# Optimization experiments

Measured on AMD Instinct MI355X. Metric: run time of the kernel, lower is better.

The kernel has to match this reference:

```python
import jax, jax.numpy as jnp
import numpy as np

B, S, D = 2, 1024, 1024      # batch, seq_len, d_model
E, K, FF = 8, 2, 2048        # num_experts, top_k, dim_feedforward


def setup_inputs() -> dict:
    key = jax.random.key(0)
    k1, k2, k3, k4 = jax.random.split(key, 4)
    x = jax.random.normal(k1, (B, S, D), dtype=jnp.float32)
    router_w = jax.random.normal(k2, (E, D), dtype=jnp.float32) * 0.02   # nn.Linear(d_model, num_experts).weight
    w1 = jax.random.normal(k3, (E, FF, D), dtype=jnp.float32) * 0.02     # per-expert nn.Linear(d, ff).weight
    w2 = jax.random.normal(k4, (E, D, FF), dtype=jnp.float32) * 0.02     # per-expert nn.Linear(ff, d).weight
    return {"x": x, "router_w": router_w, "w1": w1, "w2": w2}


def reference(x, router_w, w1, w2):
    # Router: logits -> softmax -> top-k -> renormalize
    logits = jnp.einsum('bsd,ed->bse', x, router_w)
    router_probs = jax.nn.softmax(logits, axis=-1)                       # [B,S,E]
    topk_weights, topk_indices = jax.lax.top_k(router_probs, K)          # [B,S,K]
    topk_weights = topk_weights / topk_weights.sum(axis=-1, keepdims=True)
    # Combine weight per (token, expert): sum of top-k weights routed to that expert
    combine = (jax.nn.one_hot(topk_indices, E, dtype=x.dtype) * topk_weights[..., None]).sum(axis=-2)  # [B,S,E]
    # Experts: SwiGLU-less SiLU MLP per expert, applied densely then masked by combine weights.
    h = jax.nn.silu(jnp.einsum('bsd,efd->bsef', x, w1))                  # [B,S,E,FF]
    y = jnp.einsum('bsef,edf->bsed', h, w2)                              # [B,S,E,D]
    output = jnp.einsum('bsed,bse->bsd', y, combine)                     # [B,S,D]
    return output, router_probs, topk_indices, topk_weights
```

## Files before the change

kernel.cpp:

```cpp
#include <hip/hip_runtime.h>
#include <hip/hip_bf16.h>

#define TOKENS 2048
#define DMODEL 1024
#define NEXP 8
#define TOPK 2
#define FFDIM 2048
#define MAXSLOTS 5120
#define MTILES (MAXSLOTS / 128)

typedef __bf16 bf16_t;
typedef __bf16 bf16x8 __attribute__((ext_vector_type(8)));
typedef __bf16 bf16x4 __attribute__((ext_vector_type(4)));
typedef float f32x4 __attribute__((ext_vector_type(4)));

#define OUT_PROBS (TOKENS * DMODEL)
#define OUT_IDX (OUT_PROBS + TOKENS * NEXP)
#define OUT_W (OUT_IDX + TOKENS * TOPK)

#define WS_TOKE 0
#define WS_TOKW 16384
#define WS_OFFS 32768
#define WS_ROWTOK 33024
#define WS_SLOTOF 53504
#define WS_XB 131072
#define WS_H 4325376
#define WS_Y 25296896
#define WS_WB 35782656

__device__ __forceinline__ void async16(const bf16_t* g, bf16_t* l) {
    __builtin_amdgcn_global_load_lds(
        (const __attribute__((address_space(1))) unsigned int*)g,
        (__attribute__((address_space(3))) unsigned int*)l, 16, 0, 0);
}

__global__ __launch_bounds__(256) void k_cast(const float* __restrict__ src,
                                              bf16_t* __restrict__ dst) {
    const size_t i = ((size_t)blockIdx.x * 256 + threadIdx.x) * 8;
    float4 a = *(const float4*)&src[i];
    float4 b = *(const float4*)&src[i + 4];
    bf16x8 v;
    v[0] = (bf16_t)a.x; v[1] = (bf16_t)a.y; v[2] = (bf16_t)a.z; v[3] = (bf16_t)a.w;
    v[4] = (bf16_t)b.x; v[5] = (bf16_t)b.y; v[6] = (bf16_t)b.z; v[7] = (bf16_t)b.w;
    *(bf16x8*)&dst[i] = v;
}

__global__ __launch_bounds__(256) void k_router(
        const float* __restrict__ x, const float* __restrict__ rw,
        float* __restrict__ out, int* __restrict__ tok_e, float* __restrict__ tok_w,
        bf16_t* __restrict__ xb) {
    __shared__ float s_rw[NEXP * DMODEL];
    const float4* rw4 = (const float4*)rw;
    float4* s4 = (float4*)s_rw;
#pragma unroll
    for (int i = 0; i < (NEXP * DMODEL / 4) / 256; ++i)
        s4[i * 256 + threadIdx.x] = rw4[i * 256 + threadIdx.x];
    __syncthreads();

    const int wave = threadIdx.x >> 6;
    const int lane = threadIdx.x & 63;
    const int t = blockIdx.x * 4 + wave;

    float acc[NEXP];
#pragma unroll
    for (int e = 0; e < NEXP; ++e) acc[e] = 0.f;
    const float4* xr = (const float4*)(x + (size_t)t * DMODEL);
#pragma unroll
    for (int j = 0; j < DMODEL / 256; ++j) {
        float4 xv = xr[j * 64 + lane];
        bf16x4 xc;
        xc[0] = (bf16_t)xv.x; xc[1] = (bf16_t)xv.y; xc[2] = (bf16_t)xv.z; xc[3] = (bf16_t)xv.w;
        *(bf16x4*)&xb[(size_t)t * DMODEL + (j * 64 + lane) * 4] = xc;
#pragma unroll
        for (int e = 0; e < NEXP; ++e) {
            const float4 rv = *(const float4*)&s_rw[e * DMODEL + (j * 64 + lane) * 4];
            acc[e] += xv.x * rv.x + xv.y * rv.y + xv.z * rv.z + xv.w * rv.w;
        }
    }
#pragma unroll
    for (int off = 32; off > 0; off >>= 1) {
#pragma unroll
        for (int e = 0; e < NEXP; ++e) acc[e] += __shfl_xor(acc[e], off);
    }

    if (lane == 0) {
        float m = acc[0];
#pragma unroll
        for (int e = 1; e < NEXP; ++e) m = fmaxf(m, acc[e]);
        float p[NEXP];
        float sum = 0.f;
#pragma unroll
        for (int e = 0; e < NEXP; ++e) { p[e] = expf(acc[e] - m); sum += p[e]; }
#pragma unroll
        for (int e = 0; e < NEXP; ++e) p[e] = p[e] / sum;
        int i0 = 0;
#pragma unroll
        for (int e = 1; e < NEXP; ++e) if (p[e] > p[i0]) i0 = e;
        int i1 = (i0 == 0) ? 1 : 0;
#pragma unroll
        for (int e = 0; e < NEXP; ++e) if (e != i0 && p[e] > p[i1]) i1 = e;
        float w0 = p[i0], w1 = p[i1];
        float s2 = w0 + w1;
        float w0n = w0 / s2, w1n = w1 / s2;
#pragma unroll
        for (int e = 0; e < NEXP; ++e) out[OUT_PROBS + (size_t)t * NEXP + e] = p[e];
        out[OUT_IDX + (size_t)t * TOPK + 0] = (float)i0;
        out[OUT_IDX + (size_t)t * TOPK + 1] = (float)i1;
        out[OUT_W + (size_t)t * TOPK + 0] = w0n;
        out[OUT_W + (size_t)t * TOPK + 1] = w1n;
        tok_e[t * 2 + 0] = i0;
        tok_e[t * 2 + 1] = i1;
        tok_w[t * 2 + 0] = w0n;
        tok_w[t * 2 + 1] = w1n;
    }
}

__global__ void k_finalize(const int* __restrict__ tok_e,
                           int* __restrict__ offs, int* __restrict__ row_tok,
                           int* __restrict__ slot_of) {
    __shared__ int cnt[NEXP];
    __shared__ int fill[NEXP];
    __shared__ int soff[NEXP + 1];
    const int tid = threadIdx.x;
    if (tid < NEXP) { cnt[tid] = 0; fill[tid] = 0; }
    __syncthreads();
    for (int i = tid; i < TOKENS * 2; i += 256) atomicAdd(&cnt[tok_e[i]], 1);
    __syncthreads();
    if (tid == 0) {
        int o = 0;
        for (int e = 0; e < NEXP; ++e) {
            soff[e] = o;
            o += (cnt[e] + 127) & ~127;
        }
        soff[NEXP] = o;
    }
    __syncthreads();
    if (tid <= NEXP) offs[tid] = soff[tid];
    for (int i = tid; i < MAXSLOTS; i += 256) row_tok[i] = -1;
    __syncthreads();
    for (int i = tid; i < TOKENS * 2; i += 256) {
        int e = tok_e[i];
        int pos = atomicAdd(&fill[e], 1);
        int slot = soff[e] + pos;
        row_tok[slot] = i >> 1;
        slot_of[i] = slot;
    }
}

__global__ __launch_bounds__(256, 2) void k_gemm1(
        const bf16_t* __restrict__ xb, const bf16_t* __restrict__ w1b,
        const int* __restrict__ offs, const int* __restrict__ row_tok,
        bf16_t* __restrict__ H) {
    const int m0 = blockIdx.y * 128;
    if (m0 >= offs[NEXP]) return;
    int e = 0;
    while (m0 >= offs[e + 1]) ++e;
    const int n0 = blockIdx.x * 128;

    __shared__ __align__(16) bf16_t As[2][128 * 64];
    __shared__ __align__(16) bf16_t Bs[2][128 * 64];

    const int tid = threadIdx.x;
    const int wid = tid >> 6, lane = tid & 63;
    const int wr = wid >> 1, wc = wid & 1;
    const int lr = lane & 15, ls = lane >> 4;

    const int rq = tid >> 3;
    const int jx = (tid & 7) ^ (rq & 7);
    const bf16_t* asrc[4];
    const bf16_t* bsrc[4];
#pragma unroll
    for (int q = 0; q < 4; ++q) {
        const int r = q * 32 + rq;
        int tok = row_tok[m0 + r];
        if (tok < 0) tok = 0;
        asrc[q] = xb + (size_t)tok * DMODEL + jx * 8;
        bsrc[q] = w1b + ((size_t)e * FFDIM + n0 + r) * DMODEL + jx * 8;
    }

    f32x4 acc[4][4];
#pragma unroll
    for (int mi = 0; mi < 4; ++mi)
#pragma unroll
        for (int ni = 0; ni < 4; ++ni) acc[mi][ni] = (f32x4){0.f, 0.f, 0.f, 0.f};

    const int NK = DMODEL / 64;

#define STAGE1(b, kt)                                      \
    {                                                      \
        bf16_t* Ad = &As[b][wid * 512];                    \
        bf16_t* Bd = &Bs[b][wid * 512];                    \
        _Pragma("unroll") for (int q = 0; q < 4; ++q) {    \
            async16(asrc[q] + (kt) * 64, Ad + q * 2048);   \
            async16(bsrc[q] + (kt) * 64, Bd + q * 2048);   \
        }                                                  \
    }

    int buf = 0;
    STAGE1(0, 0);
    __syncthreads();
    for (int kt = 0; kt < NK; ++kt) {
        if (kt + 1 < NK) STAGE1(buf ^ 1, kt + 1);
#pragma unroll
        for (int kk = 0; kk < 2; ++kk) {
            const int sA = ((kk << 2) + ls) ^ (lr & 7);
            bf16x8 af[4], bv[4];
#pragma unroll
            for (int mi = 0; mi < 4; ++mi)
                af[mi] = *(const bf16x8*)&As[buf][(wr * 64 + mi * 16 + lr) * 64 + sA * 8];
#pragma unroll
            for (int ni = 0; ni < 4; ++ni)
                bv[ni] = *(const bf16x8*)&Bs[buf][(wc * 64 + ni * 16 + lr) * 64 + sA * 8];
#pragma unroll
            for (int mi = 0; mi < 4; ++mi)
#pragma unroll
                for (int ni = 0; ni < 4; ++ni)
                    acc[mi][ni] = __builtin_amdgcn_mfma_f32_16x16x32_bf16(af[mi], bv[ni], acc[mi][ni], 0, 0, 0);
        }
        __syncthreads();
        buf ^= 1;
    }
#undef STAGE1

#pragma unroll
    for (int mi = 0; mi < 4; ++mi) {
        const int rowL = m0 + wr * 64 + mi * 16 + ls * 4;
#pragma unroll
        for (int ni = 0; ni < 4; ++ni) {
            const int colL = n0 + wc * 64 + ni * 16 + lr;
#pragma unroll
            for (int v = 0; v < 4; ++v) {
                float val = acc[mi][ni][v];
                H[(size_t)(rowL + v) * FFDIM + colL] = (bf16_t)(val / (1.f + expf(-val)));
            }
        }
    }
}

__global__ __launch_bounds__(256, 3) void k_gemm2(
        const bf16_t* __restrict__ H, const bf16_t* __restrict__ w2b,
        const int* __restrict__ offs, bf16_t* __restrict__ Y) {
    const int m0 = blockIdx.y * 128;
    if (m0 >= offs[NEXP]) return;
    int e = 0;
    while (m0 >= offs[e + 1]) ++e;
    const int n0 = blockIdx.x * 64;

    __shared__ __align__(16) bf16_t As[2][128 * 64];
    __shared__ __align__(16) bf16_t Bs[2][64 * 64];

    const int tid = threadIdx.x;
    const int wid = tid >> 6, lane = tid & 63;
    const int wr = wid >> 1, wc = wid & 1;
    const int lr = lane & 15, ls = lane >> 4;

    const int rq = tid >> 3;
    const int jx = (tid & 7) ^ (rq & 7);
    const bf16_t* asrc[4];
    const bf16_t* bsrc[2];
#pragma unroll
    for (int q = 0; q < 4; ++q)
        asrc[q] = H + (size_t)(m0 + q * 32 + rq) * FFDIM + jx * 8;
#pragma unroll
    for (int q = 0; q < 2; ++q)
        bsrc[q] = w2b + ((size_t)e * DMODEL + n0 + q * 32 + rq) * FFDIM + jx * 8;

    f32x4 acc[4][2];
#pragma unroll
    for (int mi = 0; mi < 4; ++mi)
#pragma unroll
        for (int ni = 0; ni < 2; ++ni) acc[mi][ni] = (f32x4){0.f, 0.f, 0.f, 0.f};

    const int NK = FFDIM / 64;

#define STAGE2(b, kt)                                      \
    {                                                      \
        bf16_t* Ad = &As[b][wid * 512];                    \
        bf16_t* Bd = &Bs[b][wid * 512];                    \
        _Pragma("unroll") for (int q = 0; q < 4; ++q)      \
            async16(asrc[q] + (kt) * 64, Ad + q * 2048);   \
        _Pragma("unroll") for (int q = 0; q < 2; ++q)      \
            async16(bsrc[q] + (kt) * 64, Bd + q * 2048);   \
    }

    int buf = 0;
    STAGE2(0, 0);
    __syncthreads();
    for (int kt = 0; kt < NK; ++kt) {
        if (kt + 1 < NK) STAGE2(buf ^ 1, kt + 1);
#pragma unroll
        for (int kk = 0; kk < 2; ++kk) {
            const int sA = ((kk << 2) + ls) ^ (lr & 7);
            bf16x8 af[4], bv[2];
#pragma unroll
            for (int mi = 0; mi < 4; ++mi)
                af[mi] = *(const bf16x8*)&As[buf][(wr * 64 + mi * 16 + lr) * 64 + sA * 8];
#pragma unroll
            for (int ni = 0; ni < 2; ++ni)
                bv[ni] = *(const bf16x8*)&Bs[buf][(wc * 32 + ni * 16 + lr) * 64 + sA * 8];
#pragma unroll
            for (int mi = 0; mi < 4; ++mi)
#pragma unroll
                for (int ni = 0; ni < 2; ++ni)
                    acc[mi][ni] = __builtin_amdgcn_mfma_f32_16x16x32_bf16(af[mi], bv[ni], acc[mi][ni], 0, 0, 0);
        }
        __syncthreads();
        buf ^= 1;
    }
#undef STAGE2

#pragma unroll
    for (int mi = 0; mi < 4; ++mi) {
        const int rowL = m0 + wr * 64 + mi * 16 + ls * 4;
#pragma unroll
        for (int ni = 0; ni < 2; ++ni) {
            const int colL = n0 + wc * 32 + ni * 16 + lr;
#pragma unroll
            for (int v = 0; v < 4; ++v)
                Y[(size_t)(rowL + v) * DMODEL + colL] = (bf16_t)acc[mi][ni][v];
        }
    }
}

__global__ __launch_bounds__(256) void k_combine(
        const bf16_t* __restrict__ Y, const int* __restrict__ slot_of,
        const float* __restrict__ tok_w, float* __restrict__ out) {
    const int t = blockIdx.x;
    const int c = threadIdx.x * 4;
    const int s0 = slot_of[t * 2 + 0], s1 = slot_of[t * 2 + 1];
    const float w0 = tok_w[t * 2 + 0], w1 = tok_w[t * 2 + 1];
    bf16x4 y0 = *(const bf16x4*)&Y[(size_t)s0 * DMODEL + c];
    bf16x4 y1 = *(const bf16x4*)&Y[(size_t)s1 * DMODEL + c];
    float4 o;
    o.x = w0 * (float)y0[0] + w1 * (float)y1[0];
    o.y = w0 * (float)y0[1] + w1 * (float)y1[1];
    o.z = w0 * (float)y0[2] + w1 * (float)y1[2];
    o.w = w0 * (float)y0[3] + w1 * (float)y1[3];
    *(float4*)&out[(size_t)t * DMODEL + c] = o;
}

extern "C" void kernel_launch(void* const* d_in, const int* in_sizes, int n_in,
                              void* d_out, int out_size, void* d_ws, size_t ws_size,
                              hipStream_t stream) {
    const float* x = (const float*)d_in[0];
    const float* rw = (const float*)d_in[1];
    const float* w1 = (const float*)d_in[2];
    const float* w2 = (const float*)d_in[3];
    float* out = (float*)d_out;
    char* ws = (char*)d_ws;

    int* tok_e = (int*)(ws + WS_TOKE);
    float* tok_w = (float*)(ws + WS_TOKW);
    int* offs = (int*)(ws + WS_OFFS);
    int* row_tok = (int*)(ws + WS_ROWTOK);
    int* slot_of = (int*)(ws + WS_SLOTOF);
    bf16_t* xb = (bf16_t*)(ws + WS_XB);
    bf16_t* H = (bf16_t*)(ws + WS_H);
    bf16_t* Yb = (bf16_t*)(ws + WS_Y);
    bf16_t* wb = (bf16_t*)(ws + WS_WB);

    const int WCAST_BLOCKS = (NEXP * FFDIM * DMODEL) / (8 * 256);

    k_router<<<TOKENS / 4, 256, 0, stream>>>(x, rw, out, tok_e, tok_w, xb);
    k_finalize<<<1, 256, 0, stream>>>(tok_e, offs, row_tok, slot_of);
    k_cast<<<WCAST_BLOCKS, 256, 0, stream>>>(w1, wb);
    k_gemm1<<<dim3(FFDIM / 128, MTILES), 256, 0, stream>>>(xb, wb, offs, row_tok, H);
    k_cast<<<WCAST_BLOCKS, 256, 0, stream>>>(w2, wb);
    k_gemm2<<<dim3(DMODEL / 64, MTILES), 256, 0, stream>>>(H, wb, offs, Yb);
    k_combine<<<TOKENS, 256, 0, stream>>>(Yb, slot_of, tok_w, out);
}
```

Measured before the change: 254.9 us.

## Fuse fp32-to-bf16 weight conversion into expert GEMM B-tile loads

Removes the separate weight cast kernels and instead has both expert GEMMs load fp32 weight tiles into registers, convert to bf16, and write them swizzled into shared memory. This avoids writing and re-reading a full bf16 copy of each weight tensor. In exchange, each M-tile re-reads fp32 weights (twice the bytes of bf16). The B path also becomes synchronous register staging with a full vmcnt wait, which adds register pressure and weakens the async pipelining.

```diff
diff --git a/kernel.cpp b/kernel.cpp
--- a/kernel.cpp
+++ b/kernel.cpp
@@ -26,7 +26,6 @@
 #define WS_XB 131072
 #define WS_H 4325376
 #define WS_Y 25296896
-#define WS_WB 35782656
 
 __device__ __forceinline__ void async16(const bf16_t* g, bf16_t* l) {
     __builtin_amdgcn_global_load_lds(
@@ -34,15 +33,11 @@
         (__attribute__((address_space(3))) unsigned int*)l, 16, 0, 0);
 }
 
-__global__ __launch_bounds__(256) void k_cast(const float* __restrict__ src,
-                                              bf16_t* __restrict__ dst) {
-    const size_t i = ((size_t)blockIdx.x * 256 + threadIdx.x) * 8;
-    float4 a = *(const float4*)&src[i];
-    float4 b = *(const float4*)&src[i + 4];
+__device__ __forceinline__ bf16x8 cvt8(float4 a, float4 b) {
     bf16x8 v;
     v[0] = (bf16_t)a.x; v[1] = (bf16_t)a.y; v[2] = (bf16_t)a.z; v[3] = (bf16_t)a.w;
     v[4] = (bf16_t)b.x; v[5] = (bf16_t)b.y; v[6] = (bf16_t)b.z; v[7] = (bf16_t)b.w;
-    *(bf16x8*)&dst[i] = v;
+    return v;
 }
 
 __global__ __launch_bounds__(256) void k_router(
@@ -148,7 +143,7 @@
 }
 
 __global__ __launch_bounds__(256, 2) void k_gemm1(
-        const bf16_t* __restrict__ xb, const bf16_t* __restrict__ w1b,
+        const bf16_t* __restrict__ xb, const float* __restrict__ w1,
         const int* __restrict__ offs, const int* __restrict__ row_tok,
         bf16_t* __restrict__ H) {
     const int m0 = blockIdx.y * 128;
@@ -168,15 +163,14 @@
     const int rq = tid >> 3;
     const int jx = (tid & 7) ^ (rq & 7);
     const bf16_t* asrc[4];
-    const bf16_t* bsrc[4];
 #pragma unroll
     for (int q = 0; q < 4; ++q) {
-        const int r = q * 32 + rq;
-        int tok = row_tok[m0 + r];
+        int tok = row_tok[m0 + q * 32 + rq];
         if (tok < 0) tok = 0;
         asrc[q] = xb + (size_t)tok * DMODEL + jx * 8;
-        bsrc[q] = w1b + ((size_t)e * FFDIM + n0 + r) * DMODEL + jx * 8;
-    }
+    }
+    const int rowB = tid >> 1, hB = tid & 1;
+    const float* brow = w1 + ((size_t)e * FFDIM + n0 + rowB) * DMODEL + hB * 32;
 
     f32x4 acc[4][4];
 #pragma unroll
@@ -185,22 +179,31 @@
         for (int ni = 0; ni < 4; ++ni) acc[mi][ni] = (f32x4){0.f, 0.f, 0.f, 0.f};
 
     const int NK = DMODEL / 64;
-
-#define STAGE1(b, kt)                                      \
-    {                                                      \
-        bf16_t* Ad = &As[b][wid * 512];                    \
-        bf16_t* Bd = &Bs[b][wid * 512];                    \
-        _Pragma("unroll") for (int q = 0; q < 4; ++q) {    \
-            async16(asrc[q] + (kt) * 64, Ad + q * 2048);   \
-            async16(bsrc[q] + (kt) * 64, Bd + q * 2048);   \
-        }                                                  \
-    }
+    float4 bb[8];
+
+#define G1_AISSUE(b, kt)                                                     \
+    _Pragma("unroll") for (int q = 0; q < 4; ++q)                            \
+        async16(asrc[q] + (kt) * 64, &As[b][wid * 512] + q * 2048);
+#define G1_BLOAD(kt)                                                         \
+    _Pragma("unroll") for (int i = 0; i < 8; ++i)                            \
+        bb[i] = *(const float4*)(brow + (kt) * 64 + i * 4);
+#define G1_BWRITE(b)                                                         \
+    _Pragma("unroll") for (int s = 0; s < 4; ++s)                            \
+        *(bf16x8*)&Bs[b][rowB * 64 + (((hB << 2) + s) ^ (rowB & 7)) * 8] =   \
+            cvt8(bb[2 * s], bb[2 * s + 1]);
+
+    G1_BLOAD(0);
+    G1_AISSUE(0, 0);
+    asm volatile("s_waitcnt vmcnt(0)" ::: "memory");
+    G1_BWRITE(0);
+    __syncthreads();
 
     int buf = 0;
-    STAGE1(0, 0);
-    __syncthreads();
     for (int kt = 0; kt < NK; ++kt) {
-        if (kt + 1 < NK) STAGE1(buf ^ 1, kt + 1);
+        if (kt + 1 < NK) {
+            G1_BLOAD(kt + 1);
+            G1_AISSUE(buf ^ 1, kt + 1);
+        }
 #pragma unroll
         for (int kk = 0; kk < 2; ++kk) {
             const int sA = ((kk << 2) + ls) ^ (lr & 7);
@@ -217,10 +220,16 @@
                 for (int ni = 0; ni < 4; ++ni)
                     acc[mi][ni] = __builtin_amdgcn_mfma_f32_16x16x32_bf16(af[mi], bv[ni], acc[mi][ni], 0, 0, 0);
         }
+        if (kt + 1 < NK) {
+            asm volatile("s_waitcnt vmcnt(0)" ::: "memory");
+            G1_BWRITE(buf ^ 1);
+        }
         __syncthreads();
         buf ^= 1;
     }
-#undef STAGE1
+#undef G1_AISSUE
+#undef G1_BLOAD
+#undef G1_BWRITE
 
 #pragma unroll
     for (int mi = 0; mi < 4; ++mi) {
@@ -238,7 +247,7 @@
 }
 
 __global__ __launch_bounds__(256, 3) void k_gemm2(
-        const bf16_t* __restrict__ H, const bf16_t* __restrict__ w2b,
+        const bf16_t* __restrict__ H, const float* __restrict__ w2,
         const int* __restrict__ offs, bf16_t* __restrict__ Y) {
     const int m0 = blockIdx.y * 128;
     if (m0 >= offs[NEXP]) return;
@@ -257,13 +266,11 @@
     const int rq = tid >> 3;
     const int jx = (tid & 7) ^ (rq & 7);
     const bf16_t* asrc[4];
-    const bf16_t* bsrc[2];
 #pragma unroll
     for (int q = 0; q < 4; ++q)
         asrc[q] = H + (size_t)(m0 + q * 32 + rq) * FFDIM + jx * 8;
-#pragma unroll
-    for (int q = 0; q < 2; ++q)
-        bsrc[q] = w2b + ((size_t)e * DMODEL + n0 + q * 32 + rq) * FFDIM + jx * 8;
+    const int rowB = tid >> 2, qB = tid & 3;
+    const float* brow = w2 + ((size_t)e * DMODEL + n0 + rowB) * FFDIM + qB * 16;
 
     f32x4 acc[4][2];
 #pragma unroll
@@ -272,22 +279,31 @@
         for (int ni = 0; ni < 2; ++ni) acc[mi][ni] = (f32x4){0.f, 0.f, 0.f, 0.f};
 
     const int NK = FFDIM / 64;
-
-#define STAGE2(b, kt)                                      \
-    {                                                      \
-        bf16_t* Ad = &As[b][wid * 512];                    \
-        bf16_t* Bd = &Bs[b][wid * 512];                    \
-        _Pragma("unroll") for (int q = 0; q < 4; ++q)      \
-            async16(asrc[q] + (kt) * 64, Ad + q * 2048);   \
-        _Pragma("unroll") for (int q = 0; q < 2; ++q)      \
-            async16(bsrc[q] + (kt) * 64, Bd + q * 2048);   \
-    }
+    float4 cb[4];
+
+#define G2_AISSUE(b, kt)                                                     \
+    _Pragma("unroll") for (int q = 0; q < 4; ++q)                            \
+        async16(asrc[q] + (kt) * 64, &As[b][wid * 512] + q * 2048);
+#define G2_BLOAD(kt)                                                         \
+    _Pragma("unroll") for (int i = 0; i < 4; ++i)                            \
+        cb[i] = *(const float4*)(brow + (kt) * 64 + i * 4);
+#define G2_BWRITE(b)                                                         \
+    _Pragma("unroll") for (int s = 0; s < 2; ++s)                            \
+        *(bf16x8*)&Bs[b][rowB * 64 + (((qB << 1) + s) ^ (rowB & 7)) * 8] =   \
+            cvt8(cb[2 * s], cb[2 * s + 1]);
+
+    G2_BLOAD(0);
+    G2_AISSUE(0, 0);
+    asm volatile("s_waitcnt vmcnt(0)" ::: "memory");
+    G2_BWRITE(0);
+    __syncthreads();
 
     int buf = 0;
-    STAGE2(0, 0);
-    __syncthreads();
     for (int kt = 0; kt < NK; ++kt) {
-        if (kt + 1 < NK) STAGE2(buf ^ 1, kt + 1);
+        if (kt + 1 < NK) {
+            G2_BLOAD(kt + 1);
+            G2_AISSUE(buf ^ 1, kt + 1);
+        }
 #pragma unroll
         for (int kk = 0; kk < 2; ++kk) {
             const int sA = ((kk << 2) + ls) ^ (lr & 7);
@@ -304,10 +320,16 @@
                 for (int ni = 0; ni < 2; ++ni)
                     acc[mi][ni] = __builtin_amdgcn_mfma_f32_16x16x32_bf16(af[mi], bv[ni], acc[mi][ni], 0, 0, 0);
         }
+        if (kt + 1 < NK) {
+            asm volatile("s_waitcnt vmcnt(0)" ::: "memory");
+            G2_BWRITE(buf ^ 1);
+        }
         __syncthreads();
         buf ^= 1;
     }
-#undef STAGE2
+#undef G2_AISSUE
+#undef G2_BLOAD
+#undef G2_BWRITE
 
 #pragma unroll
     for (int mi = 0; mi < 4; ++mi) {
@@ -357,15 +379,10 @@
     bf16_t* xb = (bf16_t*)(ws + WS_XB);
     bf16_t* H = (bf16_t*)(ws + WS_H);
     bf16_t* Yb = (bf16_t*)(ws + WS_Y);
-    bf16_t* wb = (bf16_t*)(ws + WS_WB);
-
-    const int WCAST_BLOCKS = (NEXP * FFDIM * DMODEL) / (8 * 256);
 
     k_router<<<TOKENS / 4, 256, 0, stream>>>(x, rw, out, tok_e, tok_w, xb);
     k_finalize<<<1, 256, 0, stream>>>(tok_e, offs, row_tok, slot_of);
-    k_cast<<<WCAST_BLOCKS, 256, 0, stream>>>(w1, wb);
-    k_gemm1<<<dim3(FFDIM / 128, MTILES), 256, 0, stream>>>(xb, wb, offs, row_tok, H);
-    k_cast<<<WCAST_BLOCKS, 256, 0, stream>>>(w2, wb);
-    k_gemm2<<<dim3(DMODEL / 64, MTILES), 256, 0, stream>>>(H, wb, offs, Yb);
+    k_gemm1<<<dim3(FFDIM / 128, MTILES), 256, 0, stream>>>(xb, w1, offs, row_tok, H);
+    k_gemm2<<<dim3(DMODEL / 64, MTILES), 256, 0, stream>>>(H, w2, offs, Yb);
     k_combine<<<TOKENS, 256, 0, stream>>>(Yb, slot_of, tok_w, out);
 }
```

Result: slower. 297.2 us (+16.6%).
